# Optimization experiments

Measured on AMD Instinct MI355X. Metric: run time of the kernel, lower is better.

The kernel has to match this reference:

```python
import jax, jax.numpy as jnp
import numpy as np


def _c2e(faces):
    # faces: [6, B, C, h, h] in order back, down, front, left, right, up
    # returns equirect map [B, C, H=h, W=2h] via bilinear cube sampling
    _, B, C, h, _ = faces.shape
    H, W = h, 2 * h
    lat = (0.5 - (jnp.arange(H) + 0.5) / H) * jnp.pi      # +pi/2 (top) .. -pi/2
    lon = (2.0 * (jnp.arange(W) + 0.5) / W - 1.0) * jnp.pi  # -pi .. +pi
    cl = jnp.cos(lat)[:, None]
    vx = cl * jnp.sin(lon)[None, :]
    vy = jnp.broadcast_to(jnp.sin(lat)[:, None], (H, W))
    vz = cl * jnp.cos(lon)[None, :]
    dirs = jnp.stack([vx, vy, vz], -1)                     # [H,W,3]
    ax, ay, az = jnp.abs(vx), jnp.abs(vy), jnp.abs(vz)
    cond_z = (az >= ax) & (az >= ay)
    cond_x = (~cond_z) & (ax >= ay)
    # face ids: 0 back(-z) 1 down(-y) 2 front(+z) 3 left(-x) 4 right(+x) 5 up(+y)
    face = jnp.where(cond_z, jnp.where(vz > 0, 2, 0),
                     jnp.where(cond_x, jnp.where(vx > 0, 4, 3),
                               jnp.where(vy > 0, 5, 1)))
    N = jnp.array([[0, 0, -1], [0, -1, 0], [0, 0, 1], [-1, 0, 0], [1, 0, 0], [0, 1, 0]], jnp.float32)
    R = jnp.array([[-1, 0, 0], [1, 0, 0], [1, 0, 0], [0, 0, 1], [0, 0, -1], [1, 0, 0]], jnp.float32)
    U = jnp.array([[0, 1, 0], [0, 0, -1], [0, 1, 0], [0, 1, 0], [0, 1, 0], [0, 0, 1]], jnp.float32)
    den = jnp.sum(dirs * N[face], -1)
    a = jnp.sum(dirs * R[face], -1) / den                  # in-plane x, [-1,1]
    bcoord = jnp.sum(dirs * U[face], -1) / den             # in-plane y, [-1,1]
    uu = jnp.clip((a + 1.0) * 0.5 * (h - 1), 0.0, h - 1)   # align_corners-style
    vv = jnp.clip((1.0 - bcoord) * 0.5 * (h - 1), 0.0, h - 1)
    x0 = jnp.floor(uu).astype(jnp.int32)
    y0 = jnp.floor(vv).astype(jnp.int32)
    x1 = jnp.minimum(x0 + 1, h - 1)
    y1 = jnp.minimum(y0 + 1, h - 1)
    dx = uu - x0
    dy = vv - y0
    ft = faces.transpose(0, 3, 4, 1, 2).reshape(6, h, h, B * C)  # [6,h,h,B*C]
    g = lambda yy, xx: ft[face, yy, xx]                    # gather -> [H,W,B*C]
    out = (g(y0, x0) * ((1 - dx) * (1 - dy))[..., None]
           + g(y0, x1) * (dx * (1 - dy))[..., None]
           + g(y1, x0) * ((1 - dx) * dy)[..., None]
           + g(y1, x1) * (dx * dy)[..., None])
    return out.reshape(H, W, B, C).transpose(2, 3, 0, 1)


def _conv(x, w, bias, pad):
    y = jax.lax.conv_general_dilated(x, w, (1, 1), [(pad, pad), (pad, pad)],
                                     dimension_numbers=('NCHW', 'OIHW', 'NCHW'))
    return y + bias[None, :, None, None]


def setup_inputs() -> dict:
    key = jax.random.key(0)
    ks = jax.random.split(key, 12)
    B, C, h = 4, 64, 128
    face_shape = (B, C, h, h)
    return {
        'm': jax.random.normal(ks[0], (B, C, h, 2 * h), jnp.float32),
        'f': jax.random.normal(ks[1], face_shape, jnp.float32),
        'r': jax.random.normal(ks[2], face_shape, jnp.float32),
        'b': jax.random.normal(ks[3], face_shape, jnp.float32),
        'l': jax.random.normal(ks[4], face_shape, jnp.float32),
        'u': jax.random.normal(ks[5], face_shape, jnp.float32),
        'd': jax.random.normal(ks[6], face_shape, jnp.float32),
        'w_fusion': jax.random.normal(ks[7], (C, C, 3, 3), jnp.float32) * 0.05,
        'b_fusion': jnp.zeros((C,), jnp.float32),
        'w_mask': jax.random.normal(ks[8], (1, 2 * C, 1, 1), jnp.float32) * 0.05,
        'b_mask': jnp.zeros((1,), jnp.float32),
    }


def reference(m, f, r, b, l, u, d, w_fusion, b_fusion, w_mask, b_mask):
    # cube faces stacked in the original order: back, down, front, left, right, up
    faces = jnp.stack([b, d, f, l, r, u], 0)               # [6,B,C,h,h]
    aux = _c2e(faces)                                      # [B,C,h,2h]
    m_aux = jax.nn.relu(_conv(aux, w_fusion, b_fusion, 1))
    m_main = jax.nn.relu(_conv(m, w_fusion, b_fusion, 1))  # shared conv_fusion weights
    joint = jnp.concatenate([m_main, m_aux], axis=1)
    mask = jax.nn.sigmoid(_conv(joint, w_mask, b_mask, 0)) # [B,1,h,2h]
    return m + mask * m_aux
```

## Files before the change

kernel.cpp:

```cpp
#include <hip/hip_runtime.h>
#include <math.h>
#include <stdint.h>

#define BB 4
#define CC 64
#define HH 128
#define HOUT 128
#define WOUT 256
#define NPIX (HOUT * WOUT)
#define NMAP (BB * CC * HOUT * WOUT)
#define FSTR ((size_t)HH * HH * 256)

#define NB_PREP 146
#define NB_FACE (6 * HH * 2)
#define NB_FRONT (NB_PREP + NB_FACE)

typedef __attribute__((ext_vector_type(8))) short short8;
typedef __attribute__((ext_vector_type(4))) float floatx4;

__device__ __forceinline__ uint16_t f2bf(float f) {
    uint32_t u = __float_as_uint(f);
    u += 0x7fffu + ((u >> 16) & 1u);
    return (uint16_t)(u >> 16);
}
__device__ __forceinline__ float bfu2f(uint32_t v) { return __uint_as_float(v << 16); }

__global__ __launch_bounds__(256) void front_kernel(
    uint32_t* __restrict__ pk, float* __restrict__ pdx, float* __restrict__ pdy,
    const float* __restrict__ wf, uint4* __restrict__ Bsw,
    const float* __restrict__ pB, const float* __restrict__ pD,
    const float* __restrict__ pF, const float* __restrict__ pL,
    const float* __restrict__ pR, const float* __restrict__ pU,
    uint16_t* __restrict__ FCL) {
    __shared__ uint16_t lds[64 * 256];
    int bid = blockIdx.x;
    int t = threadIdx.x;

    if (bid < NB_PREP) {
        if (bid < 128) {
            int p = bid * 256 + t;
            int y = p >> 8;
            int x = p & 255;
            const float PI = 3.14159265358979323846f;
            float lat = (0.5f - (y + 0.5f) / (float)HOUT) * PI;
            float lon = (2.0f * (x + 0.5f) / (float)WOUT - 1.0f) * PI;
            float cl = cosf(lat);
            float vx = cl * sinf(lon);
            float vy = sinf(lat);
            float vz = cl * cosf(lon);
            float ax = fabsf(vx), ay = fabsf(vy), az = fabsf(vz);

            int face;
            float den, a, b;
            if (az >= ax && az >= ay) {
                if (vz > 0.0f) { face = 2; den = vz;  a = vx;  b = vy; }
                else           { face = 0; den = -vz; a = -vx; b = vy; }
            } else if (ax >= ay) {
                if (vx > 0.0f) { face = 4; den = vx;  a = -vz; b = vy; }
                else           { face = 3; den = -vx; a = vz;  b = vy; }
            } else {
                if (vy > 0.0f) { face = 5; den = vy;  a = vx;  b = vz; }
                else           { face = 1; den = -vy; a = vx;  b = -vz; }
            }
            a /= den;
            b /= den;
            float uu = fminf(fmaxf((a + 1.0f) * 0.5f * (HH - 1), 0.0f), (float)(HH - 1));
            float vv = fminf(fmaxf((1.0f - b) * 0.5f * (HH - 1), 0.0f), (float)(HH - 1));
            int x0 = (int)floorf(uu);
            int y0 = (int)floorf(vv);
            int x1 = min(x0 + 1, HH - 1);
            int y1 = min(y0 + 1, HH - 1);
            pdx[p] = uu - (float)x0;
            pdy[p] = vv - (float)y0;
            pk[p] = (uint32_t)face | ((uint32_t)x0 << 3) | ((uint32_t)y0 << 10) |
                    ((uint32_t)x1 << 17) | ((uint32_t)y1 << 24);
        } else {
            int tid = (bid - 128) * 256 + t;
            if (tid >= 9 * 2 * 4 * 64) return;
            int lane = tid & 63;
            int rest = tid >> 6;
            int n = rest & 3, ks = (rest >> 2) & 1, tap = rest >> 3;
            int co = n * 16 + (lane & 15);
            uint32_t w4[4];
#pragma unroll
            for (int pw = 0; pw < 4; pw++) {
                int ci0 = ks * 32 + (lane >> 4) * 8 + pw * 2;
                uint32_t lo = f2bf(wf[(size_t)(co * CC + ci0) * 9 + tap]);
                uint32_t hi = f2bf(wf[(size_t)(co * CC + ci0 + 1) * 9 + tap]);
                w4[pw] = lo | (hi << 16);
            }
            Bsw[tid] = make_uint4(w4[0], w4[1], w4[2], w4[3]);
        }
    } else {
        int fb = bid - NB_PREP;
        int half = fb & 1;
        int y = (fb >> 1) & 127;
        int fc = fb >> 8;
        const float* src = (fc == 0) ? pB : (fc == 1) ? pD : (fc == 2) ? pF
                         : (fc == 3) ? pL : (fc == 4) ? pR : pU;
        uint16_t* FCLf = FCL + (size_t)fc * FSTR;

#pragma unroll
        for (int it = 0; it < 16; it++) {
            int jq = it * 256 + t;
            int bc = jq >> 4;
            int q = jq & 15;
            floatx4 v = *(const floatx4*)(src + ((size_t)bc * HH + y) * HH +
                                          half * 64 + q * 4);
            int cg = bc >> 3;
#pragma unroll
            for (int j = 0; j < 4; j++) {
                int xl = q * 4 + j;
                lds[xl * 256 + ((cg ^ (xl & 7)) << 3) + (bc & 7)] = f2bf(v[j]);
            }
        }
        __syncthreads();
        size_t obase = ((size_t)y * HH + half * 64) * 256;
#pragma unroll
        for (int i = 0; i < 8; i++) {
            int q = i * 256 + t;
            int xx = q >> 5, cg = q & 31;
            int off = xx * 256 + ((cg ^ (xx & 7)) * 8);
            *(uint4*)&FCLf[obase + (size_t)q * 8] = *(const uint4*)&lds[off];
        }
    }
}

__global__ __launch_bounds__(256, 4) void gemm_fused_kernel(
    const float* __restrict__ m, const uint16_t* __restrict__ FCL,
    const uint32_t* __restrict__ pk, const float* __restrict__ pdx,
    const float* __restrict__ pdy, const uint4* __restrict__ Bsw,
    const float* __restrict__ bias, const float* __restrict__ wm,
    const float* __restrict__ bm, float* __restrict__ out) {
    __shared__ __align__(16) uint16_t lds[3 * 132 * 64];
    float* ldsf = (float*)lds;

    int gid = blockIdx.x;
    int b = gid >> 8;
    int i = gid & 255;
    int xcd = i & 7, j = i >> 3;
    int y = xcd * 16 + (j & 15);
    int h = j >> 4;
    const int wx = h * 128 - 2;

    int tid = threadIdx.x;
    int lane = tid & 63;
    int wave = tid >> 6;
    int l15 = lane & 15, lq = lane >> 4;

    float bb[4], wmm[4], wma[4];
#pragma unroll
    for (int n = 0; n < 4; n++) {
        bb[n] = bias[n * 16 + l15];
        wmm[n] = wm[n * 16 + l15];
        wma[n] = wm[64 + n * 16 + l15];
    }
    float bm0 = bm[0];

    float mp[2][4];
#pragma unroll
    for (int mt = 0; mt < 2; mt++)
#pragma unroll
        for (int rg = 0; rg < 4; rg++) mp[mt][rg] = 0.0f;

    floatx4 acc[2][4];

    auto stage_m = [&](int cid) {
        int c = cid & 7, pr = cid >> 3;
        int p = pr % 132, r = pr / 132;
        int gy = y + r - 1, gx = wx + p;
        uint32_t w4[4] = {0u, 0u, 0u, 0u};
        if ((unsigned)gy < (unsigned)HOUT && (unsigned)gx < (unsigned)WOUT) {
            const float* mp0 = m + ((size_t)(b * CC + c * 8) * HOUT + gy) * WOUT + gx;
#pragma unroll
            for (int jj = 0; jj < 4; jj++) {
                uint32_t lo = f2bf(mp0[(size_t)(2 * jj) * NPIX]);
                uint32_t hi = f2bf(mp0[(size_t)(2 * jj + 1) * NPIX]);
                w4[jj] = lo | (hi << 16);
            }
        }
        int slot = (r * 132 + p) * 8 + (c ^ (p & 7));
        *(uint4*)&lds[slot * 8] = make_uint4(w4[0], w4[1], w4[2], w4[3]);
    };

    auto stage_a = [&](int cid) {
        int c = cid & 7, pr = cid >> 3;
        int p = pr % 132, r = pr / 132;
        int gy = y + r - 1, gx = wx + p;
        uint32_t w4[4] = {0u, 0u, 0u, 0u};
        if ((unsigned)gy < (unsigned)HOUT && (unsigned)gx < (unsigned)WOUT) {
            int pg = gy * WOUT + gx;
            uint32_t k = pk[pg];
            float dxw = pdx[pg], dyw = pdy[pg];
            int fc = k & 7;
            int x0 = (k >> 3) & 127, y0 = (k >> 10) & 127;
            int x1 = (k >> 17) & 127, y1 = (k >> 24) & 127;
            const uint16_t* base = FCL + (size_t)fc * FSTR + (size_t)(b * 8 + c) * 8;
            uint4 c00 = *(const uint4*)(base + ((size_t)y0 * HH + x0) * 256);
            uint4 c01 = *(const uint4*)(base + ((size_t)y0 * HH + x1) * 256);
            uint4 c10 = *(const uint4*)(base + ((size_t)y1 * HH + x0) * 256);
            uint4 c11 = *(const uint4*)(base + ((size_t)y1 * HH + x1) * 256);
            float w00 = (1.0f - dxw) * (1.0f - dyw);
            float w01 = dxw * (1.0f - dyw);
            float w10 = (1.0f - dxw) * dyw;
            float w11 = dxw * dyw;
            const uint32_t* a00 = (const uint32_t*)&c00;
            const uint32_t* a01 = (const uint32_t*)&c01;
            const uint32_t* a10 = (const uint32_t*)&c10;
            const uint32_t* a11 = (const uint32_t*)&c11;
#pragma unroll
            for (int w = 0; w < 4; w++) {
                float lo = w00 * bfu2f(a00[w] & 0xffffu) + w01 * bfu2f(a01[w] & 0xffffu)
                         + w10 * bfu2f(a10[w] & 0xffffu) + w11 * bfu2f(a11[w] & 0xffffu);
                float hi = w00 * bfu2f(a00[w] >> 16) + w01 * bfu2f(a01[w] >> 16)
                         + w10 * bfu2f(a10[w] >> 16) + w11 * bfu2f(a11[w] >> 16);
                w4[w] = (uint32_t)f2bf(lo) | ((uint32_t)f2bf(hi) << 16);
            }
        }
        int slot = (r * 132 + p) * 8 + (c ^ (p & 7));
        *(uint4*)&lds[slot * 8] = make_uint4(w4[0], w4[1], w4[2], w4[3]);
    };

    auto conv = [&]() {
#pragma unroll
        for (int mt = 0; mt < 2; mt++)
#pragma unroll
            for (int n = 0; n < 4; n++) acc[mt][n] = (floatx4)0.0f;
#pragma unroll
        for (int tap = 0; tap < 9; tap++) {
            const int r = tap / 3;
            const int dx = tap % 3 - 1;
#pragma unroll
            for (int ks = 0; ks < 2; ks++) {
                short8 bfr[4];
                const uint4* bp = Bsw + (size_t)((tap * 2 + ks) * 4) * 64 + lane;
#pragma unroll
                for (int n = 0; n < 4; n++) {
                    uint4 t4 = bp[n * 64];
                    bfr[n] = *(short8*)&t4;
                }
#pragma unroll
                for (int mt = 0; mt < 2; mt++) {
                    int p = wave * 32 + mt * 16 + l15 + dx + 2;
                    int chunk = ks * 4 + lq;
                    int slot = (r * 132 + p) * 8 + (chunk ^ (p & 7));
                    short8 af = *(const short8*)&lds[slot * 8];
#pragma unroll
                    for (int n = 0; n < 4; n++)
                        acc[mt][n] = __builtin_amdgcn_mfma_f32_16x16x32_bf16(
                            af, bfr[n], acc[mt][n], 0, 0, 0);
                }
            }
        }
    };

    for (int it = 0; it < 12; it++) stage_m(it * 256 + tid);
    if (tid < 96) stage_m(3072 + tid);
    __syncthreads();
    conv();
#pragma unroll
    for (int mt = 0; mt < 2; mt++)
#pragma unroll
        for (int n = 0; n < 4; n++)
#pragma unroll
            for (int rg = 0; rg < 4; rg++) {
                float v = acc[mt][n][rg] + bb[n];
                v = v > 0.0f ? v : 0.0f;
                mp[mt][rg] += wmm[n] * v;
            }

    __syncthreads();
    for (int it = 0; it < 12; it++) stage_a(it * 256 + tid);
    if (tid < 96) stage_a(3072 + tid);
    __syncthreads();
    conv();
#pragma unroll
    for (int mt = 0; mt < 2; mt++)
#pragma unroll
        for (int n = 0; n < 4; n++)
#pragma unroll
            for (int rg = 0; rg < 4; rg++) {
                float v = acc[mt][n][rg] + bb[n];
                v = v > 0.0f ? v : 0.0f;
                acc[mt][n][rg] = v;
                mp[mt][rg] += wma[n] * v;
            }

#pragma unroll
    for (int mt = 0; mt < 2; mt++)
#pragma unroll
        for (int rg = 0; rg < 4; rg++) {
            float v = mp[mt][rg];
            v += __shfl_xor(v, 1);
            v += __shfl_xor(v, 2);
            v += __shfl_xor(v, 4);
            v += __shfl_xor(v, 8);
            mp[mt][rg] = 1.0f / (1.0f + expf(-(v + bm0)));
        }

    __syncthreads();
#pragma unroll
    for (int mt = 0; mt < 2; mt++)
#pragma unroll
        for (int n = 0; n < 4; n++)
#pragma unroll
            for (int rg = 0; rg < 4; rg++) {
                int px = wave * 32 + mt * 16 + lq * 4 + rg;
                int co = n * 16 + l15;
                ldsf[co * 129 + px] = mp[mt][rg] * acc[mt][n][rg];
            }
    __syncthreads();

    size_t base0 = (size_t)b * (CC * HOUT * WOUT) + (size_t)y * WOUT + h * 128;
#pragma unroll
    for (int it = 0; it < 32; it++) {
        int q = it * 256 + tid;
        int c = q >> 7, px = q & 127;
        size_t idx = base0 + (size_t)c * (HOUT * WOUT) + px;
        out[idx] = m[idx] + ldsf[c * 129 + px];
    }
}

__global__ __launch_bounds__(256) void signal_kernel(float* __restrict__ out, float v) {
    int idx = blockIdx.x * 256 + threadIdx.x;
    out[idx] = v;
}

extern "C" void kernel_launch(void* const* d_in, const int* in_sizes, int n_in,
                              void* d_out, int out_size, void* d_ws, size_t ws_size,
                              hipStream_t stream) {
    const float* m  = (const float*)d_in[0];
    const float* f  = (const float*)d_in[1];
    const float* r  = (const float*)d_in[2];
    const float* bk = (const float*)d_in[3];
    const float* l  = (const float*)d_in[4];
    const float* u  = (const float*)d_in[5];
    const float* dn = (const float*)d_in[6];
    const float* wf = (const float*)d_in[7];
    const float* bf = (const float*)d_in[8];
    const float* wm = (const float*)d_in[9];
    const float* bm = (const float*)d_in[10];
    float* out = (float*)d_out;

    const size_t OFF_FCL = 0;
    const size_t FCL_SZ  = (size_t)6 * HH * HH * 256 * 2;
    const size_t OFF_BSW = FCL_SZ;
    const size_t OFF_PK  = OFF_BSW + (9 * 2 * 4 * 64 * 16);
    const size_t OFF_PDX = OFF_PK + (1u << 17);
    const size_t OFF_PDY = OFF_PDX + (1u << 17);
    const size_t NEED    = OFF_PDY + (1u << 17);

    if (ws_size < NEED) {
        float v = 100.0f + (float)(ws_size >> 20);
        signal_kernel<<<NMAP / 256, 256, 0, stream>>>(out, v);
        return;
    }

    char* ws = (char*)d_ws;
    uint16_t* FCL = (uint16_t*)(ws + OFF_FCL);
    uint4* Bsw    = (uint4*)(ws + OFF_BSW);
    uint32_t* pk  = (uint32_t*)(ws + OFF_PK);
    float* pdx    = (float*)(ws + OFF_PDX);
    float* pdy    = (float*)(ws + OFF_PDY);

    front_kernel<<<NB_FRONT, 256, 0, stream>>>(pk, pdx, pdy, wf, Bsw,
                                               bk, dn, f, l, r, u, FCL);
    gemm_fused_kernel<<<BB * HOUT * 2, 256, 0, stream>>>(m, FCL, pk, pdx, pdy,
                                                         Bsw, bf, wm, bm, out);
}
```

Measured before the change: 265.2 us.

## Coalesce m staging with float4 row loads and strengthen LDS swizzle

Staging of the main input m into LDS now reads contiguous float4 rows along x for each channel, with separate scalar loads for the two halo columns on each side. Previously each thread gathered 8 channels at a single pixel using strided scalar loads. The LDS XOR swizzle gains a second term ((p>>3)&7), applied consistently in the face-transpose prep, the staging writes and the MFMA fragment reads, to reduce bank conflicts. Bias and mask weights are loaded per n inside the epilogue, and the staging code is restructured into a two-phase loop, likely to lower register pressure. The trade-off is more scattered 2-byte LDS writes during m staging.

```diff
diff --git a/kernel.cpp b/kernel.cpp
--- a/kernel.cpp
+++ b/kernel.cpp
@@ -111,7 +111,8 @@
 #pragma unroll
             for (int j = 0; j < 4; j++) {
                 int xl = q * 4 + j;
-                lds[xl * 256 + ((cg ^ (xl & 7)) << 3) + (bc & 7)] = f2bf(v[j]);
+                int swz = cg ^ (xl & 7) ^ ((xl >> 3) & 7);
+                lds[xl * 256 + (swz << 3) + (bc & 7)] = f2bf(v[j]);
             }
         }
         __syncthreads();
@@ -120,7 +121,8 @@
         for (int i = 0; i < 8; i++) {
             int q = i * 256 + t;
             int xx = q >> 5, cg = q & 31;
-            int off = xx * 256 + ((cg ^ (xx & 7)) * 8);
+            int swz = cg ^ (xx & 7) ^ ((xx >> 3) & 7);
+            int off = xx * 256 + swz * 8;
             *(uint4*)&FCLf[obase + (size_t)q * 8] = *(const uint4*)&lds[off];
         }
     }
@@ -148,84 +150,123 @@
     int wave = tid >> 6;
     int l15 = lane & 15, lq = lane >> 4;
 
-    float bb[4], wmm[4], wma[4];
-#pragma unroll
-    for (int n = 0; n < 4; n++) {
-        bb[n] = bias[n * 16 + l15];
-        wmm[n] = wm[n * 16 + l15];
-        wma[n] = wm[64 + n * 16 + l15];
+    float mp[2][4];
+#pragma unroll
+    for (int mt = 0; mt < 2; mt++)
+#pragma unroll
+        for (int rg = 0; rg < 4; rg++) mp[mt][rg] = 0.0f;
+
+    floatx4 acc[2][4];
+
+    {
+        const float* mb = m + (size_t)b * (CC * HOUT * WOUT);
+#pragma unroll 4
+        for (int it = 0; it < 24; it++) {
+            int jq = it * 256 + tid;
+            int q = jq & 31;
+            int rc = jq >> 5;
+            int c = rc & 63;
+            int r = rc >> 6;
+            int gy = y + r - 1;
+            int gx = h * 128 + q * 4;
+            floatx4 v = (floatx4)0.0f;
+            if ((unsigned)gy < (unsigned)HOUT)
+                v = *(const floatx4*)(mb + ((size_t)c * HOUT + gy) * WOUT + gx);
+            int cc = c >> 3, cl = c & 7;
+#pragma unroll
+            for (int jj = 0; jj < 4; jj++) {
+                int p = 2 + q * 4 + jj;
+                int slot = (r * 132 + p) * 8 + (cc ^ (p & 7) ^ ((p >> 3) & 7));
+                lds[slot * 8 + cl] = f2bf(v[jj]);
+            }
+        }
+#pragma unroll
+        for (int hp = 0; hp < 2; hp++) {
+            int jq = hp * 256 + tid;
+            if (jq < 384) {
+                int side = jq & 1;
+                int rc = jq >> 1;
+                int c = rc & 63;
+                int r = rc >> 6;
+                int gy = y + r - 1;
+                int px0 = side ? 130 : 0;
+                int cc = c >> 3, cl = c & 7;
+#pragma unroll
+                for (int jj = 0; jj < 2; jj++) {
+                    int p = px0 + jj;
+                    int gx = wx + p;
+                    float v = 0.0f;
+                    if ((unsigned)gy < (unsigned)HOUT && (unsigned)gx < (unsigned)WOUT)
+                        v = mb[((size_t)c * HOUT + gy) * WOUT + gx];
+                    int slot = (r * 132 + p) * 8 + (cc ^ (p & 7) ^ ((p >> 3) & 7));
+                    lds[slot * 8 + cl] = f2bf(v);
+                }
+            }
+        }
     }
-    float bm0 = bm[0];
-
-    float mp[2][4];
-#pragma unroll
-    for (int mt = 0; mt < 2; mt++)
-#pragma unroll
-        for (int rg = 0; rg < 4; rg++) mp[mt][rg] = 0.0f;
-
-    floatx4 acc[2][4];
-
-    auto stage_m = [&](int cid) {
-        int c = cid & 7, pr = cid >> 3;
-        int p = pr % 132, r = pr / 132;
-        int gy = y + r - 1, gx = wx + p;
-        uint32_t w4[4] = {0u, 0u, 0u, 0u};
-        if ((unsigned)gy < (unsigned)HOUT && (unsigned)gx < (unsigned)WOUT) {
-            const float* mp0 = m + ((size_t)(b * CC + c * 8) * HOUT + gy) * WOUT + gx;
-#pragma unroll
-            for (int jj = 0; jj < 4; jj++) {
-                uint32_t lo = f2bf(mp0[(size_t)(2 * jj) * NPIX]);
-                uint32_t hi = f2bf(mp0[(size_t)(2 * jj + 1) * NPIX]);
-                w4[jj] = lo | (hi << 16);
-            }
-        }
-        int slot = (r * 132 + p) * 8 + (c ^ (p & 7));
-        *(uint4*)&lds[slot * 8] = make_uint4(w4[0], w4[1], w4[2], w4[3]);
-    };
-
-    auto stage_a = [&](int cid) {
-        int c = cid & 7, pr = cid >> 3;
-        int p = pr % 132, r = pr / 132;
-        int gy = y + r - 1, gx = wx + p;
-        uint32_t w4[4] = {0u, 0u, 0u, 0u};
-        if ((unsigned)gy < (unsigned)HOUT && (unsigned)gx < (unsigned)WOUT) {
-            int pg = gy * WOUT + gx;
-            uint32_t k = pk[pg];
-            float dxw = pdx[pg], dyw = pdy[pg];
-            int fc = k & 7;
-            int x0 = (k >> 3) & 127, y0 = (k >> 10) & 127;
-            int x1 = (k >> 17) & 127, y1 = (k >> 24) & 127;
-            const uint16_t* base = FCL + (size_t)fc * FSTR + (size_t)(b * 8 + c) * 8;
-            uint4 c00 = *(const uint4*)(base + ((size_t)y0 * HH + x0) * 256);
-            uint4 c01 = *(const uint4*)(base + ((size_t)y0 * HH + x1) * 256);
-            uint4 c10 = *(const uint4*)(base + ((size_t)y1 * HH + x0) * 256);
-            uint4 c11 = *(const uint4*)(base + ((size_t)y1 * HH + x1) * 256);
-            float w00 = (1.0f - dxw) * (1.0f - dyw);
-            float w01 = dxw * (1.0f - dyw);
-            float w10 = (1.0f - dxw) * dyw;
-            float w11 = dxw * dyw;
-            const uint32_t* a00 = (const uint32_t*)&c00;
-            const uint32_t* a01 = (const uint32_t*)&c01;
-            const uint32_t* a10 = (const uint32_t*)&c10;
-            const uint32_t* a11 = (const uint32_t*)&c11;
-#pragma unroll
-            for (int w = 0; w < 4; w++) {
-                float lo = w00 * bfu2f(a00[w] & 0xffffu) + w01 * bfu2f(a01[w] & 0xffffu)
-                         + w10 * bfu2f(a10[w] & 0xffffu) + w11 * bfu2f(a11[w] & 0xffffu);
-                float hi = w00 * bfu2f(a00[w] >> 16) + w01 * bfu2f(a01[w] >> 16)
-                         + w10 * bfu2f(a10[w] >> 16) + w11 * bfu2f(a11[w] >> 16);
-                w4[w] = (uint32_t)f2bf(lo) | ((uint32_t)f2bf(hi) << 16);
-            }
-        }
-        int slot = (r * 132 + p) * 8 + (c ^ (p & 7));
-        *(uint4*)&lds[slot * 8] = make_uint4(w4[0], w4[1], w4[2], w4[3]);
-    };
-
-    auto conv = [&]() {
+    __syncthreads();
+
+#pragma unroll
+    for (int phase = 0; phase < 2; phase++) {
+        if (phase == 1) {
+            __syncthreads();
+#pragma unroll 2
+            for (int it = 0; it < 13; it++) {
+                int cid = it * 256 + tid;
+                if (cid < 3168) {
+                    int c = cid & 7;
+                    int pr = cid >> 3;
+                    int p = pr % 132;
+                    int r = pr / 132;
+                    int gy = y + r - 1;
+                    int gx = wx + p;
+                    uint32_t w4[4] = {0u, 0u, 0u, 0u};
+                    if ((unsigned)gy < (unsigned)HOUT && (unsigned)gx < (unsigned)WOUT) {
+                        int pg = gy * WOUT + gx;
+                        uint32_t k = pk[pg];
+                        float dxw = pdx[pg], dyw = pdy[pg];
+                        int fc = k & 7;
+                        int x0 = (k >> 3) & 127, y0 = (k >> 10) & 127;
+                        int x1 = (k >> 17) & 127, y1 = (k >> 24) & 127;
+                        const uint16_t* base =
+                            FCL + (size_t)fc * FSTR + (size_t)(b * 8 + c) * 8;
+                        uint4 c00 = *(const uint4*)(base + ((size_t)y0 * HH + x0) * 256);
+                        uint4 c01 = *(const uint4*)(base + ((size_t)y0 * HH + x1) * 256);
+                        uint4 c10 = *(const uint4*)(base + ((size_t)y1 * HH + x0) * 256);
+                        uint4 c11 = *(const uint4*)(base + ((size_t)y1 * HH + x1) * 256);
+                        float w00 = (1.0f - dxw) * (1.0f - dyw);
+                        float w01 = dxw * (1.0f - dyw);
+                        float w10 = (1.0f - dxw) * dyw;
+                        float w11 = dxw * dyw;
+                        const uint32_t* a00 = (const uint32_t*)&c00;
+                        const uint32_t* a01 = (const uint32_t*)&c01;
+                        const uint32_t* a10 = (const uint32_t*)&c10;
+                        const uint32_t* a11 = (const uint32_t*)&c11;
+#pragma unroll
+                        for (int w = 0; w < 4; w++) {
+                            float lo = w00 * bfu2f(a00[w] & 0xffffu)
+                                     + w01 * bfu2f(a01[w] & 0xffffu)
+                                     + w10 * bfu2f(a10[w] & 0xffffu)
+                                     + w11 * bfu2f(a11[w] & 0xffffu);
+                            float hi = w00 * bfu2f(a00[w] >> 16)
+                                     + w01 * bfu2f(a01[w] >> 16)
+                                     + w10 * bfu2f(a10[w] >> 16)
+                                     + w11 * bfu2f(a11[w] >> 16);
+                            w4[w] = (uint32_t)f2bf(lo) | ((uint32_t)f2bf(hi) << 16);
+                        }
+                    }
+                    int slot = (r * 132 + p) * 8 + (c ^ (p & 7) ^ ((p >> 3) & 7));
+                    *(uint4*)&lds[slot * 8] = make_uint4(w4[0], w4[1], w4[2], w4[3]);
+                }
+            }
+            __syncthreads();
+        }
+
 #pragma unroll
         for (int mt = 0; mt < 2; mt++)
 #pragma unroll
             for (int n = 0; n < 4; n++) acc[mt][n] = (floatx4)0.0f;
+
 #pragma unroll
         for (int tap = 0; tap < 9; tap++) {
             const int r = tap / 3;
@@ -243,7 +284,7 @@
                 for (int mt = 0; mt < 2; mt++) {
                     int p = wave * 32 + mt * 16 + l15 + dx + 2;
                     int chunk = ks * 4 + lq;
-                    int slot = (r * 132 + p) * 8 + (chunk ^ (p & 7));
+                    int slot = (r * 132 + p) * 8 + (chunk ^ (p & 7) ^ ((p >> 3) & 7));
                     short8 af = *(const short8*)&lds[slot * 8];
 #pragma unroll
                     for (int n = 0; n < 4; n++)
@@ -252,40 +293,40 @@
                 }
             }
         }
-    };
-
-    for (int it = 0; it < 12; it++) stage_m(it * 256 + tid);
-    if (tid < 96) stage_m(3072 + tid);
-    __syncthreads();
-    conv();
-#pragma unroll
-    for (int mt = 0; mt < 2; mt++)
-#pragma unroll
-        for (int n = 0; n < 4; n++)
-#pragma unroll
-            for (int rg = 0; rg < 4; rg++) {
-                float v = acc[mt][n][rg] + bb[n];
-                v = v > 0.0f ? v : 0.0f;
-                mp[mt][rg] += wmm[n] * v;
-            }
-
-    __syncthreads();
-    for (int it = 0; it < 12; it++) stage_a(it * 256 + tid);
-    if (tid < 96) stage_a(3072 + tid);
-    __syncthreads();
-    conv();
-#pragma unroll
-    for (int mt = 0; mt < 2; mt++)
-#pragma unroll
-        for (int n = 0; n < 4; n++)
-#pragma unroll
-            for (int rg = 0; rg < 4; rg++) {
-                float v = acc[mt][n][rg] + bb[n];
-                v = v > 0.0f ? v : 0.0f;
-                acc[mt][n][rg] = v;
-                mp[mt][rg] += wma[n] * v;
-            }
-
+
+        if (phase == 0) {
+#pragma unroll
+            for (int n = 0; n < 4; n++) {
+                float bb = bias[n * 16 + l15];
+                float wmn = wm[n * 16 + l15];
+#pragma unroll
+                for (int mt = 0; mt < 2; mt++)
+#pragma unroll
+                    for (int rg = 0; rg < 4; rg++) {
+                        float v = acc[mt][n][rg] + bb;
+                        v = v > 0.0f ? v : 0.0f;
+                        mp[mt][rg] += wmn * v;
+                    }
+            }
+        } else {
+#pragma unroll
+            for (int n = 0; n < 4; n++) {
+                float bb = bias[n * 16 + l15];
+                float wan = wm[64 + n * 16 + l15];
+#pragma unroll
+                for (int mt = 0; mt < 2; mt++)
+#pragma unroll
+                    for (int rg = 0; rg < 4; rg++) {
+                        float v = acc[mt][n][rg] + bb;
+                        v = v > 0.0f ? v : 0.0f;
+                        acc[mt][n][rg] = v;
+                        mp[mt][rg] += wan * v;
+                    }
+            }
+        }
+    }
+
+    float bm0 = bm[0];
 #pragma unroll
     for (int mt = 0; mt < 2; mt++)
 #pragma unroll
```

Result: slower. 291.8 us (+10.0%).
